# Kernel tuning notes

Measured on AMD Instinct MI355X. Metric: run time of the kernel, lower is better.

Reference implementation:

```python
import jax, jax.numpy as jnp
import numpy as np

B, S, D, H = 16, 2048, 1024, 1024
WINDOW = 2


def setup_inputs() -> dict:
    key = jax.random.key(0)
    k1, k2 = jax.random.split(key)
    X = jax.random.normal(k1, (B, S, D), dtype=jnp.float32)
    hidden = jnp.zeros((B, H), dtype=jnp.float32)  # initial hidden state (None -> zeros, same math)
    # Linear(window*input_size, 3*hidden_size) weights (torch layout: [out, in])
    W = jax.random.normal(k2, (3 * H, WINDOW * D), dtype=jnp.float32) * (1.0 / np.sqrt(WINDOW * D))
    b = jnp.zeros((3 * H,), dtype=jnp.float32)
    return {"X": X, "hidden": hidden, "W": W, "b": b}


def reference(X, hidden, W, b):
    # X: (B, S, D) -> (S, B, D) as in torch permute(1, 0, 2)
    Xs = jnp.transpose(X, (1, 0, 2))
    # window == 2: concat current token with previous token (zero-padded at t=0)
    Xm1 = jnp.concatenate([jnp.zeros_like(Xs[:1]), Xs[:-1]], axis=0)
    source = jnp.concatenate([Xs, Xm1], axis=2)  # (S, B, 2D)
    Y = jnp.einsum('sbd,hd->sbh', source, W) + b  # (S, B, 3H)
    Z, F, O = jnp.split(Y, 3, axis=2)
    Z = jnp.tanh(Z)
    F = jax.nn.sigmoid(F)

    # ForgetMult: c_t = f_t * z_t + (1 - f_t) * c_{t-1}  (diagonal linear recurrence)
    def step(c, fz):
        f, z = fz
        c = f * z + (1.0 - f) * c
        return c, c

    c_last, C = jax.lax.scan(step, hidden, (F, Z))  # C: (S, B, H)
    Hout = jax.nn.sigmoid(O) * C  # output gate (QRNN-fo)
    return Hout, c_last
```

## Files before the change

kernel.cpp:

```cpp
#include <hip/hip_runtime.h>
#include <hip/hip_bf16.h>
#include <cstdint>
#include <cstddef>


typedef _Float16 f16;
typedef _Float16 f16x4 __attribute__((ext_vector_type(4)));
typedef _Float16 f16x8 __attribute__((ext_vector_type(8)));
typedef float f32x4 __attribute__((ext_vector_type(4)));

#define Bb 16
#define Ss 2048
#define Dd 1024
#define Hh 1024
#define Nn (3 * Hh)
#define Kk (2 * Dd)
#define BH (Bb * Hh)

__device__ __forceinline__ void gl_lds16(const void* g, void* l) {
  __builtin_amdgcn_global_load_lds(
      (const __attribute__((address_space(1))) void*)g,
      (__attribute__((address_space(3))) void*)l, 16, 0, 0);
}

__global__ void cvt_f32_f16(const float* __restrict__ in, f16* __restrict__ out, int n4) {
  int i = blockIdx.x * blockDim.x + threadIdx.x;
  if (i < n4) {
    const float4 v = ((const float4*)in)[i];
    f16x4 h;
    h[0] = (f16)v.x; h[1] = (f16)v.y; h[2] = (f16)v.z; h[3] = (f16)v.w;
    ((f16x4*)out)[i] = h;
  }
}

__global__ __launch_bounds__(256, 4)
void gemm_gates(const f16* __restrict__ Xh,
                const f16* __restrict__ Wh,
                const float* __restrict__ bias,
                const f16* __restrict__ zblk,
                f16* __restrict__ Zg, f16* __restrict__ Fg, f16* __restrict__ Og) {
  __shared__ __align__(16) f16 As[128 * 64];
  __shared__ __align__(16) f16 Bs[128 * 64];

  const int tid  = threadIdx.x;
  const int wave = tid >> 6;
  const int lane = tid & 63;
  const int bn = blockIdx.x;
  const int bm = blockIdx.y;
  const int m0 = bm * 128;
  const int n0 = bn * 128;

  const int wm = (wave >> 1) * 64;
  const int wn = (wave & 1) * 64;
  const int r  = lane & 15;
  const int q  = lane >> 4;

  const int srl  = lane >> 3;
  const int sseg = ((lane & 7) ^ srl) * 8;

  int as_[4], ab_[4];
#pragma unroll
  for (int i = 0; i < 4; ++i) {
    int mrow = m0 + wave * 32 + i * 8 + srl;
    as_[i] = mrow >> 4;
    ab_[i] = mrow & 15;
  }

  f32x4 acc[4][4];
#pragma unroll
  for (int i = 0; i < 4; ++i)
#pragma unroll
    for (int j = 0; j < 4; ++j)
      acc[i][j] = {0.f, 0.f, 0.f, 0.f};

  for (int kt = 0; kt < 32; ++kt) {
    const int kf = kt * 64;
    __syncthreads();
#pragma unroll
    for (int i = 0; i < 4; ++i) {
      const int row0 = wave * 32 + i * 8;
      const f16* gp;
      if (kf < 1024) {
        gp = Xh + (size_t)ab_[i] * (Ss * Dd) + as_[i] * Dd + kf + sseg;
      } else if (as_[i] > 0) {
        gp = Xh + (size_t)ab_[i] * (Ss * Dd) + (as_[i] - 1) * Dd + (kf - 1024) + sseg;
      } else {
        gp = zblk + sseg;
      }
      gl_lds16(gp, &As[row0 * 64]);
    }
#pragma unroll
    for (int i = 0; i < 4; ++i) {
      const int row0 = wave * 32 + i * 8;
      const f16* gp = Wh + (size_t)(n0 + row0 + srl) * Kk + kf + sseg;
      gl_lds16(gp, &Bs[row0 * 64]);
    }
    __syncthreads();
#pragma unroll
    for (int kk = 0; kk < 64; kk += 32) {
      f16x8 af[4], bf[4];
#pragma unroll
      for (int mi = 0; mi < 4; ++mi) {
        const int row = wm + mi * 16 + r;
        const int seg = ((kk >> 3) + q) ^ (row & 7);
        af[mi] = *(const f16x8*)&As[row * 64 + seg * 8];
      }
#pragma unroll
      for (int ni = 0; ni < 4; ++ni) {
        const int row = wn + ni * 16 + r;
        const int seg = ((kk >> 3) + q) ^ (row & 7);
        bf[ni] = *(const f16x8*)&Bs[row * 64 + seg * 8];
      }
#pragma unroll
      for (int mi = 0; mi < 4; ++mi)
#pragma unroll
        for (int ni = 0; ni < 4; ++ni)
          acc[mi][ni] =
              __builtin_amdgcn_mfma_f32_16x16x32_f16(af[mi], bf[ni], acc[mi][ni], 0, 0, 0);
    }
  }

  const int gate = n0 >> 10;
  f16* gp_out = (gate == 0) ? Zg : ((gate == 1) ? Fg : Og);
#pragma unroll
  for (int ni = 0; ni < 4; ++ni) {
    const int gcol = n0 + wn + ni * 16 + r;
    const int h = gcol & 1023;
    const float bv = bias[gcol];
#pragma unroll
    for (int mi = 0; mi < 4; ++mi) {
#pragma unroll
      for (int reg = 0; reg < 4; ++reg) {
        const int grow = m0 + wm + mi * 16 + q * 4 + reg;
        const int s = grow >> 4, bb = grow & 15;
        const float y = acc[mi][ni][reg] + bv;
        float v;
        if (gate == 0) v = 2.f / (1.f + __expf(-2.f * y)) - 1.f;
        else           v = 1.f / (1.f + __expf(-y));
        gp_out[(size_t)s * BH + bb * Hh + h] = (f16)v;
      }
    }
  }
}

__global__ __launch_bounds__(64, 1)
void scan_fused(const f16* __restrict__ Zg, const f16* __restrict__ Fg,
                const f16* __restrict__ Og, const float* __restrict__ hidden,
                float* __restrict__ out) {
  const int g = blockIdx.x * 64 + threadIdx.x;
  float c = hidden[g];

  constexpr int U = 32;
  f16 z0[U], f0[U], o0[U], z1[U], f1[U], o1[U];

#pragma unroll
  for (int i = 0; i < U; ++i) {
    z0[i] = Zg[(size_t)i * BH + g];
    f0[i] = Fg[(size_t)i * BH + g];
    o0[i] = Og[(size_t)i * BH + g];
  }

  for (int t = 0; t < Ss; t += 2 * U) {
    if (t + U < Ss) {
#pragma unroll
      for (int i = 0; i < U; ++i) {
        z1[i] = Zg[(size_t)(t + U + i) * BH + g];
        f1[i] = Fg[(size_t)(t + U + i) * BH + g];
        o1[i] = Og[(size_t)(t + U + i) * BH + g];
      }
    }
#pragma unroll
    for (int i = 0; i < U; ++i) {
      const float z = (float)z0[i], f = (float)f0[i], o = (float)o0[i];
      c = fmaf(f, z - c, c);
      out[(size_t)(t + i) * BH + g] = o * c;
    }
    if (t + 2 * U < Ss) {
#pragma unroll
      for (int i = 0; i < U; ++i) {
        z0[i] = Zg[(size_t)(t + 2 * U + i) * BH + g];
        f0[i] = Fg[(size_t)(t + 2 * U + i) * BH + g];
        o0[i] = Og[(size_t)(t + 2 * U + i) * BH + g];
      }
    }
#pragma unroll
    for (int i = 0; i < U; ++i) {
      const float z = (float)z1[i], f = (float)f1[i], o = (float)o1[i];
      c = fmaf(f, z - c, c);
      out[(size_t)(t + U + i) * BH + g] = o * c;
    }
  }
  out[(size_t)Ss * BH + g] = c;
}

extern "C" void kernel_launch(void* const* d_in, const int* in_sizes, int n_in,
                              void* d_out, int out_size, void* d_ws, size_t ws_size,
                              hipStream_t stream) {
  const float* X      = (const float*)d_in[0];
  const float* hidden = (const float*)d_in[1];
  const float* W      = (const float*)d_in[2];
  const float* bias   = (const float*)d_in[3];
  float* out = (float*)d_out;

  char* ws = (char*)d_ws;
  f16* zblk = (f16*)ws;
  f16* Wh = (f16*)(ws + 256);
  f16* Xh = (f16*)(ws + 256 + 12582912);
  f16* Zg = (f16*)(ws + 256 + 12582912 + 67108864);
  f16* Fg = (f16*)(ws + 256 + 12582912 + 2 * 67108864);
  f16* Og = (f16*)(ws + 256 + 12582912 + 3 * 67108864);

  hipMemsetAsync(zblk, 0, 256, stream);

  {
    int n4 = (Nn * Kk) / 4;
    cvt_f32_f16<<<(n4 + 255) / 256, 256, 0, stream>>>(W, Wh, n4);
  }
  {
    int n4 = (Bb * Ss * Dd) / 4;
    cvt_f32_f16<<<(n4 + 255) / 256, 256, 0, stream>>>(X, Xh, n4);
  }
  gemm_gates<<<dim3(24, 256), 256, 0, stream>>>(Xh, Wh, bias, zblk, Zg, Fg, Og);
  scan_fused<<<256, 64, 0, stream>>>(Zg, Fg, Og, hidden, out);
}
```

Measured before the change: 783.7 us.

## Replace serial forget-mult scan with chunked three-pass parallel scan

The single sequential scan over 2048 timesteps, launched with only 256 single-wave blocks, is replaced by three kernels. The first computes a per-chunk affine summary (product of 1-f and local state) over 16 chunks of 128 steps, the second combines the chunk carries sequentially, and the third replays each chunk from its carry-in while writing outputs. This exposes 16x more parallelism, and each thread now handles two hidden units through f16x2 loads. The cost is reading Z and F twice and adding small partial buffers.

Result: faster. 735.6 us (-6.1%).

```diff
diff --git a/kernel.cpp b/kernel.cpp
--- a/kernel.cpp
+++ b/kernel.cpp
@@ -5,6 +5,7 @@
 
 
 typedef _Float16 f16;
+typedef _Float16 f16x2 __attribute__((ext_vector_type(2)));
 typedef _Float16 f16x4 __attribute__((ext_vector_type(4)));
 typedef _Float16 f16x8 __attribute__((ext_vector_type(8)));
 typedef float f32x4 __attribute__((ext_vector_type(4)));
@@ -16,6 +17,9 @@
 #define Nn (3 * Hh)
 #define Kk (2 * Dd)
 #define BH (Bb * Hh)
+#define NCH 16
+#define CL 128
+#define NQ 8192
 
 __device__ __forceinline__ void gl_lds16(const void* g, void* l) {
   __builtin_amdgcn_global_load_lds(
@@ -143,54 +147,119 @@
   }
 }
 
-__global__ __launch_bounds__(64, 1)
-void scan_fused(const f16* __restrict__ Zg, const f16* __restrict__ Fg,
-                const f16* __restrict__ Og, const float* __restrict__ hidden,
+__global__ __launch_bounds__(256, 4)
+void chunk_reduce(const f16* __restrict__ Zg, const f16* __restrict__ Fg,
+                  float* __restrict__ Apart, float* __restrict__ Bpart) {
+  const int idx = blockIdx.x * 256 + threadIdx.x;
+  const int q = idx & (NQ - 1);
+  const int p = idx >> 13;
+  const int base = p * CL;
+  constexpr int U = 16;
+  f16x2 zb[2][U], fb[2][U];
+#pragma unroll
+  for (int i = 0; i < U; ++i) {
+    zb[0][i] = ((const f16x2*)(Zg + (size_t)(base + i) * BH))[q];
+    fb[0][i] = ((const f16x2*)(Fg + (size_t)(base + i) * BH))[q];
+  }
+  float a0 = 1.f, a1 = 1.f, c0 = 0.f, c1 = 0.f;
+  for (int t = 0; t < CL; t += 2 * U) {
+#pragma unroll
+    for (int i = 0; i < U; ++i) {
+      zb[1][i] = ((const f16x2*)(Zg + (size_t)(base + t + U + i) * BH))[q];
+      fb[1][i] = ((const f16x2*)(Fg + (size_t)(base + t + U + i) * BH))[q];
+    }
+#pragma unroll
+    for (int i = 0; i < U; ++i) {
+      const float f0 = (float)fb[0][i][0], f1 = (float)fb[0][i][1];
+      const float z0 = (float)zb[0][i][0], z1 = (float)zb[0][i][1];
+      c0 = fmaf(f0, z0 - c0, c0); c1 = fmaf(f1, z1 - c1, c1);
+      a0 *= 1.f - f0; a1 *= 1.f - f1;
+    }
+    if (t + 2 * U < CL) {
+#pragma unroll
+      for (int i = 0; i < U; ++i) {
+        zb[0][i] = ((const f16x2*)(Zg + (size_t)(base + t + 2 * U + i) * BH))[q];
+        fb[0][i] = ((const f16x2*)(Fg + (size_t)(base + t + 2 * U + i) * BH))[q];
+      }
+    }
+#pragma unroll
+    for (int i = 0; i < U; ++i) {
+      const float f0 = (float)fb[1][i][0], f1 = (float)fb[1][i][1];
+      const float z0 = (float)zb[1][i][0], z1 = (float)zb[1][i][1];
+      c0 = fmaf(f0, z0 - c0, c0); c1 = fmaf(f1, z1 - c1, c1);
+      a0 *= 1.f - f0; a1 *= 1.f - f1;
+    }
+  }
+  ((float2*)Apart)[(size_t)p * NQ + q] = make_float2(a0, a1);
+  ((float2*)Bpart)[(size_t)p * NQ + q] = make_float2(c0, c1);
+}
+
+__global__ __launch_bounds__(256)
+void chunk_scan(const float* __restrict__ Apart, const float* __restrict__ Bpart,
+                const float* __restrict__ hidden, float* __restrict__ Cin,
                 float* __restrict__ out) {
-  const int g = blockIdx.x * 64 + threadIdx.x;
-  float c = hidden[g];
-
-  constexpr int U = 32;
-  f16 z0[U], f0[U], o0[U], z1[U], f1[U], o1[U];
-
+  const int q = blockIdx.x * 256 + threadIdx.x;
+  float2 c = ((const float2*)hidden)[q];
+#pragma unroll
+  for (int p = 0; p < NCH; ++p) {
+    ((float2*)Cin)[(size_t)p * NQ + q] = c;
+    const float2 a = ((const float2*)Apart)[(size_t)p * NQ + q];
+    const float2 b = ((const float2*)Bpart)[(size_t)p * NQ + q];
+    c.x = fmaf(a.x, c.x, b.x);
+    c.y = fmaf(a.y, c.y, b.y);
+  }
+  ((float2*)(out + (size_t)Ss * BH))[q] = c;
+}
+
+__global__ __launch_bounds__(256, 4)
+void chunk_apply(const f16* __restrict__ Zg, const f16* __restrict__ Fg,
+                 const f16* __restrict__ Og, const float* __restrict__ Cin,
+                 float* __restrict__ out) {
+  const int idx = blockIdx.x * 256 + threadIdx.x;
+  const int q = idx & (NQ - 1);
+  const int p = idx >> 13;
+  const int base = p * CL;
+  constexpr int U = 16;
+  f16x2 zb[2][U], fb[2][U], ob[2][U];
 #pragma unroll
   for (int i = 0; i < U; ++i) {
-    z0[i] = Zg[(size_t)i * BH + g];
-    f0[i] = Fg[(size_t)i * BH + g];
-    o0[i] = Og[(size_t)i * BH + g];
-  }
-
-  for (int t = 0; t < Ss; t += 2 * U) {
-    if (t + U < Ss) {
+    zb[0][i] = ((const f16x2*)(Zg + (size_t)(base + i) * BH))[q];
+    fb[0][i] = ((const f16x2*)(Fg + (size_t)(base + i) * BH))[q];
+    ob[0][i] = ((const f16x2*)(Og + (size_t)(base + i) * BH))[q];
+  }
+  float2 c = ((const float2*)Cin)[(size_t)p * NQ + q];
+  for (int t = 0; t < CL; t += 2 * U) {
+#pragma unroll
+    for (int i = 0; i < U; ++i) {
+      zb[1][i] = ((const f16x2*)(Zg + (size_t)(base + t + U + i) * BH))[q];
+      fb[1][i] = ((const f16x2*)(Fg + (size_t)(base + t + U + i) * BH))[q];
+      ob[1][i] = ((const f16x2*)(Og + (size_t)(base + t + U + i) * BH))[q];
+    }
+#pragma unroll
+    for (int i = 0; i < U; ++i) {
+      const float f0 = (float)fb[0][i][0], f1 = (float)fb[0][i][1];
+      const float z0 = (float)zb[0][i][0], z1 = (float)zb[0][i][1];
+      c.x = fmaf(f0, z0 - c.x, c.x); c.y = fmaf(f1, z1 - c.y, c.y);
+      ((float2*)(out + (size_t)(base + t + i) * BH))[q] =
+          make_float2((float)ob[0][i][0] * c.x, (float)ob[0][i][1] * c.y);
+    }
+    if (t + 2 * U < CL) {
 #pragma unroll
       for (int i = 0; i < U; ++i) {
-        z1[i] = Zg[(size_t)(t + U + i) * BH + g];
-        f1[i] = Fg[(size_t)(t + U + i) * BH + g];
-        o1[i] = Og[(size_t)(t + U + i) * BH + g];
-      }
-    }
-#pragma unroll
-    for (int i = 0; i < U; ++i) {
-      const float z = (float)z0[i], f = (float)f0[i], o = (float)o0[i];
-      c = fmaf(f, z - c, c);
-      out[(size_t)(t + i) * BH + g] = o * c;
-    }
-    if (t + 2 * U < Ss) {
-#pragma unroll
-      for (int i = 0; i < U; ++i) {
-        z0[i] = Zg[(size_t)(t + 2 * U + i) * BH + g];
-        f0[i] = Fg[(size_t)(t + 2 * U + i) * BH + g];
-        o0[i] = Og[(size_t)(t + 2 * U + i) * BH + g];
-      }
-    }
-#pragma unroll
-    for (int i = 0; i < U; ++i) {
-      const float z = (float)z1[i], f = (float)f1[i], o = (float)o1[i];
-      c = fmaf(f, z - c, c);
-      out[(size_t)(t + U + i) * BH + g] = o * c;
-    }
-  }
-  out[(size_t)Ss * BH + g] = c;
+        zb[0][i] = ((const f16x2*)(Zg + (size_t)(base + t + 2 * U + i) * BH))[q];
+        fb[0][i] = ((const f16x2*)(Fg + (size_t)(base + t + 2 * U + i) * BH))[q];
+        ob[0][i] = ((const f16x2*)(Og + (size_t)(base + t + 2 * U + i) * BH))[q];
+      }
+    }
+#pragma unroll
+    for (int i = 0; i < U; ++i) {
+      const float f0 = (float)fb[1][i][0], f1 = (float)fb[1][i][1];
+      const float z0 = (float)zb[1][i][0], z1 = (float)zb[1][i][1];
+      c.x = fmaf(f0, z0 - c.x, c.x); c.y = fmaf(f1, z1 - c.y, c.y);
+      ((float2*)(out + (size_t)(base + t + U + i) * BH))[q] =
+          make_float2((float)ob[1][i][0] * c.x, (float)ob[1][i][1] * c.y);
+    }
+  }
 }
 
 extern "C" void kernel_launch(void* const* d_in, const int* in_sizes, int n_in,
@@ -209,6 +278,9 @@
   f16* Zg = (f16*)(ws + 256 + 12582912 + 67108864);
   f16* Fg = (f16*)(ws + 256 + 12582912 + 2 * 67108864);
   f16* Og = (f16*)(ws + 256 + 12582912 + 3 * 67108864);
+  float* Apart = (float*)(ws + 256 + 12582912 + 4 * 67108864);
+  float* Bpart = Apart + NCH * BH;
+  float* Cin   = Bpart + NCH * BH;
 
   hipMemsetAsync(zblk, 0, 256, stream);
 
@@ -221,5 +293,7 @@
     cvt_f32_f16<<<(n4 + 255) / 256, 256, 0, stream>>>(X, Xh, n4);
   }
   gemm_gates<<<dim3(24, 256), 256, 0, stream>>>(Xh, Wh, bias, zblk, Zg, Fg, Og);
-  scan_fused<<<256, 64, 0, stream>>>(Zg, Fg, Og, hidden, out);
-}
+  chunk_reduce<<<(NCH * NQ) / 256, 256, 0, stream>>>(Zg, Fg, Apart, Bpart);
+  chunk_scan<<<NQ / 256, 256, 0, stream>>>(Apart, Bpart, hidden, Cin, out);
+  chunk_apply<<<(NCH * NQ) / 256, 256, 0, stream>>>(Zg, Fg, Og, Cin, out);
+}
```
